# Kernel tuning notes

Hardware: AMD Instinct MI355X
Metric: run time of the kernel (lower is better)

Reference implementation:

```python
import jax, jax.numpy as jnp
import numpy as np

E = 8        # num_experts
TOPK = 2     # num_experts_per_tok
H = 2048     # hidden_size
I = 1024     # intermediate_size (c_fc outputs 2*I because is_glu)
STD = 0.02


def setup_inputs() -> dict:
    key = jax.random.key(0)
    k1, k2, k3, k4 = jax.random.split(key, 4)
    return {
        "x": jax.random.normal(k1, (4, 2048, H), jnp.float32),
        "w_gate": jax.random.normal(k2, (E, H), jnp.float32) * STD,
        "w_fc": jax.random.normal(k3, (E, 2 * I, H), jnp.float32) * STD,
        "w_proj": jax.random.normal(k4, (E, H, I), jnp.float32) * STD,
    }


def reference(x, w_gate, w_fc, w_proj):
    orig_shape = x.shape
    xf = x.reshape(-1, H)                      # [T, H]
    T = xf.shape[0]

    # routing
    router_logits = xf @ w_gate.T              # [T, E]
    top_vals, top_idx = jax.lax.top_k(router_logits, TOPK)   # [T, K]
    router_weights = jax.nn.softmax(top_vals.astype(jnp.float32), axis=-1).astype(x.dtype)

    # combine weights: [T, E], zero for unselected experts (top-k indices are distinct)
    combine = jnp.zeros((T, E), x.dtype).at[jnp.arange(T)[:, None], top_idx].set(router_weights)

    # per-expert FFN; equivalent to sort/scatter grouped GEMM since unselected
    # tokens get zero combine weight. scan over the small fixed expert axis
    # keeps peak memory to one [T, 2I] intermediate.
    def body(y, ewc):
        wfc_e, wproj_e, c_e = ewc              # [2I,H], [H,I], [T]
        h = xf @ wfc_e.T                       # [T, 2I]
        a, b = jnp.split(h, 2, axis=-1)
        h = jax.nn.silu(a) * b                 # GLU: [T, I]
        y = y + c_e[:, None] * (h @ wproj_e.T)
        return y, None

    y0 = jnp.zeros_like(xf)
    y, _ = jax.lax.scan(body, y0, (w_fc, w_proj, combine.T))
    return y.reshape(orig_shape), router_logits
```

## Files before the change

kernel.cpp:

```cpp
#include <hip/hip_runtime.h>
#include <hip/hip_bf16.h>
#include <stdint.h>

#define T_TOK 8192
#define HID   2048
#define IM    1024
#define NE    8

typedef __attribute__((ext_vector_type(8))) short bf16x8;
typedef __attribute__((ext_vector_type(4))) float f32x4;

__device__ __forceinline__ void gload16(void* lds, const void* g) {
  __builtin_amdgcn_global_load_lds((const __attribute__((address_space(1))) char*)g,
                                   (__attribute__((address_space(3))) char*)lds, 16, 0, 0);
}

__device__ __forceinline__ ushort f2b(float f) {
  union { float f; uint32_t u; } c; c.f = f;
  uint32_t u = c.u;
  return (ushort)((u + 0x7FFFu + ((u >> 16) & 1u)) >> 16);
}

#define MFMA16(a, b, c) __builtin_amdgcn_mfma_f32_16x16x32_bf16((a), (b), (c), 0, 0, 0)

__global__ void cast_w_kernel(const float* __restrict__ wfc, const float* __restrict__ wproj,
                              ushort* __restrict__ wfcb, ushort* __restrict__ wpb) {
  const int NFC4 = NE * 2 * IM * HID / 4;
  const int NPJ4 = NE * HID * IM / 4;
  int i = blockIdx.x * blockDim.x + threadIdx.x;
  int stride = gridDim.x * blockDim.x;
  for (; i < NFC4 + NPJ4; i += stride) {
    const float4* s; ushort4* d; int k;
    if (i < NFC4) { s = (const float4*)wfc;   d = (ushort4*)wfcb; k = i; }
    else          { s = (const float4*)wproj; d = (ushort4*)wpb;  k = i - NFC4; }
    float4 v = s[k];
    ushort4 o;
    o.x = f2b(v.x); o.y = f2b(v.y); o.z = f2b(v.z); o.w = f2b(v.w);
    d[k] = o;
  }
}

__global__ __launch_bounds__(256) void router_kernel(
    const float* __restrict__ x, const float* __restrict__ wg,
    float* __restrict__ logits_out, ushort* __restrict__ xb,
    int4* __restrict__ recI, float2* __restrict__ recW,
    int* __restrict__ counts2) {
  int wid = threadIdx.x >> 6, lane = threadIdx.x & 63;
  int tok = blockIdx.x * 4 + wid;
  if (tok >= T_TOK) return;
  const float4* xr = (const float4*)(x + (size_t)tok * HID);
  float4 xv[8];
#pragma unroll
  for (int j = 0; j < 8; ++j) xv[j] = xr[j * 64 + lane];
  ushort4* xbr = (ushort4*)(xb + (size_t)tok * HID);
#pragma unroll
  for (int j = 0; j < 8; ++j) {
    ushort4 o;
    o.x = f2b(xv[j].x); o.y = f2b(xv[j].y); o.z = f2b(xv[j].z); o.w = f2b(xv[j].w);
    xbr[j * 64 + lane] = o;
  }
  float lf[NE];
#pragma unroll
  for (int e = 0; e < NE; ++e) {
    const float4* wrow = (const float4*)(wg + (size_t)e * HID);
    double acc = 0.0;
#pragma unroll
    for (int j = 0; j < 8; ++j) {
      float4 w4 = wrow[j * 64 + lane];
      acc += (double)xv[j].x * w4.x + (double)xv[j].y * w4.y +
             (double)xv[j].z * w4.z + (double)xv[j].w * w4.w;
    }
#pragma unroll
    for (int off = 32; off; off >>= 1) acc += __shfl_xor(acc, off);
    lf[e] = (float)acc;
  }
  if (lane == 0) {
#pragma unroll
    for (int e = 0; e < NE; ++e) logits_out[(size_t)tok * NE + e] = lf[e];
    int i1 = 0;
#pragma unroll
    for (int e = 1; e < NE; ++e) if (lf[e] > lf[i1]) i1 = e;
    int i2 = -1;
#pragma unroll
    for (int e = 0; e < NE; ++e) {
      if (e == i1) continue;
      if (i2 < 0 || lf[e] > lf[i2]) i2 = e;
    }
    float t = expf(lf[i2] - lf[i1]);
    float w1 = 1.0f / (1.0f + t);
    float w2 = t / (1.0f + t);
    int s1 = atomicAdd(&counts2[i1 * 2 + 0], 1);
    int s2 = atomicAdd(&counts2[i2 * 2 + 1], 1);
    recI[tok] = make_int4(i1, s1, i2, s2);
    recW[tok] = make_float2(w1, w2);
  }
}

__global__ void scan_kernel(const int* __restrict__ counts2, int* __restrict__ offs2,
                            int* __restrict__ ecnt, int* __restrict__ eoff) {
  int s = 0;
  for (int b = 0; b < 2 * NE; ++b) { offs2[b] = s; s += counts2[b]; }
  offs2[2 * NE] = s;
  for (int e = 0; e < NE; ++e) {
    eoff[e] = offs2[2 * e];
    ecnt[e] = counts2[2 * e] + counts2[2 * e + 1];
  }
}

__global__ void scatter_kernel(const int4* __restrict__ recI, const float2* __restrict__ recW,
                               const int* __restrict__ offs2,
                               int* __restrict__ tok_id, float* __restrict__ aw) {
  int t = blockIdx.x * blockDim.x + threadIdx.x;
  if (t >= T_TOK) return;
  int4 r = recI[t]; float2 w = recW[t];
  int p1 = offs2[r.x * 2 + 0] + r.y; tok_id[p1] = t; aw[p1] = w.x;
  int p2 = offs2[r.z * 2 + 1] + r.w; tok_id[p2] = t; aw[p2] = w.y;
}


__global__ __launch_bounds__(512, 2) void gemm1_kernel(
    const ushort* __restrict__ xb, const ushort* __restrict__ wfcb,
    const int* __restrict__ tok_id, const float* __restrict__ aw,
    const int* __restrict__ ecnt, const int* __restrict__ eoff,
    ushort* __restrict__ hglu) {
  int bid = blockIdx.x;
  int e = bid >> 9;
  int rt = (bid >> 3) & 63;
  int ct = bid & 7;
  int cnt = ecnt[e];
  if (cnt == 0 || rt * 256 >= cnt) return;
  int off = eoff[e];
  int tid = threadIdx.x;

  __shared__ ushort lds[4][512 * 32];

  int sslot[4]; const ushort* gsrc[4];
#pragma unroll
  for (int l = 0; l < 4; ++l) {
    int s = l * 512 + tid;
    int lrow = s >> 2, qs = s & 3;
    int gq = qs ^ ((lrow >> 1) & 3);
    sslot[l] = s * 8;
    if (l < 2) {
      int slotr = rt * 256 + lrow;
      if (slotr >= cnt) slotr = cnt - 1;
      gsrc[l] = xb + (size_t)tok_id[off + slotr] * HID + gq * 8;
    } else if (l == 2) {
      int fcr = e * 2048 + ct * 128 + (lrow - 256);
      gsrc[l] = wfcb + (size_t)fcr * HID + gq * 8;
    } else {
      int fcr = e * 2048 + 1024 + ct * 128 + (lrow - 384);
      gsrc[l] = wfcb + (size_t)fcr * HID + gq * 8;
    }
  }

  int wid = tid >> 6, lane = tid & 63;
  int wr = wid >> 2, wc = wid & 3;
  int q = lane >> 4, r = lane & 15;

  int offA[8], offBa[2], offBb[2];
#pragma unroll
  for (int m = 0; m < 8; ++m) {
    int lrow = wr * 128 + m * 16 + r;
    offA[m] = lrow * 32 + ((q ^ ((lrow >> 1) & 3)) << 3);
  }
#pragma unroll
  for (int n = 0; n < 2; ++n) {
    int lr1 = 256 + wc * 32 + n * 16 + r;
    offBa[n] = lr1 * 32 + ((q ^ ((lr1 >> 1) & 3)) << 3);
    int lr2 = 384 + wc * 32 + n * 16 + r;
    offBb[n] = lr2 * 32 + ((q ^ ((lr2 >> 1) & 3)) << 3);
  }

  f32x4 accA[8][2] = {}; f32x4 accB[8][2] = {};
  const int NT = HID / 32;

#define G1_STAGE(bufi, t, l) gload16(&lds[bufi][sslot[l]], gsrc[l] + (size_t)(t) * 32)
#pragma unroll
  for (int t = 0; t < 3; ++t) {
    G1_STAGE(t, t, 0); G1_STAGE(t, t, 1); G1_STAGE(t, t, 2); G1_STAGE(t, t, 3);
  }
  asm volatile("s_waitcnt vmcnt(8)" ::: "memory");
  __builtin_amdgcn_s_barrier();

  for (int t = 0; t < NT; ++t) {
    int cur = t & 3;
    const ushort* Bv = &lds[cur][0];
    int nb = (t + 3) & 3;
    bool pf = (t + 3) < NT;
    bf16x8 ba0 = *(const bf16x8*)&Bv[offBa[0]];
    bf16x8 ba1 = *(const bf16x8*)&Bv[offBa[1]];
    bf16x8 bb0 = *(const bf16x8*)&Bv[offBb[0]];
    bf16x8 bb1 = *(const bf16x8*)&Bv[offBb[1]];
    bf16x8 af[4];
#pragma unroll
    for (int m = 0; m < 4; ++m) af[m] = *(const bf16x8*)&Bv[offA[m]];
    if (pf) { G1_STAGE(nb, t + 3, 0); G1_STAGE(nb, t + 3, 1); }
    __builtin_amdgcn_s_barrier();
    __builtin_amdgcn_s_setprio(1);
#pragma unroll
    for (int m = 0; m < 4; ++m) {
      accA[m][0] = MFMA16(af[m], ba0, accA[m][0]);
      accA[m][1] = MFMA16(af[m], ba1, accA[m][1]);
      accB[m][0] = MFMA16(af[m], bb0, accB[m][0]);
      accB[m][1] = MFMA16(af[m], bb1, accB[m][1]);
    }
    __builtin_amdgcn_s_setprio(0);
    __builtin_amdgcn_s_barrier();
#pragma unroll
    for (int m = 0; m < 4; ++m) af[m] = *(const bf16x8*)&Bv[offA[4 + m]];
    if (pf) { G1_STAGE(nb, t + 3, 2); G1_STAGE(nb, t + 3, 3); }
    __builtin_amdgcn_s_barrier();
    __builtin_amdgcn_s_setprio(1);
#pragma unroll
    for (int m = 0; m < 4; ++m) {
      accA[4 + m][0] = MFMA16(af[m], ba0, accA[4 + m][0]);
      accA[4 + m][1] = MFMA16(af[m], ba1, accA[4 + m][1]);
      accB[4 + m][0] = MFMA16(af[m], bb0, accB[4 + m][0]);
      accB[4 + m][1] = MFMA16(af[m], bb1, accB[4 + m][1]);
    }
    __builtin_amdgcn_s_setprio(0);
    if (t < NT - 1) {
      if (t + 3 < NT)      asm volatile("s_waitcnt vmcnt(8)" ::: "memory");
      else if (t + 2 < NT) asm volatile("s_waitcnt vmcnt(4)" ::: "memory");
      else                 asm volatile("s_waitcnt vmcnt(0)" ::: "memory");
      __builtin_amdgcn_s_barrier();
    }
  }

#pragma unroll
  for (int m = 0; m < 8; ++m) {
#pragma unroll
    for (int j = 0; j < 4; ++j) {
      int slot = rt * 256 + wr * 128 + m * 16 + q * 4 + j;
      if (slot >= cnt) continue;
      float w = aw[off + slot];
      size_t rp = (size_t)(off + slot) * IM + ct * 128 + wc * 32 + r;
#pragma unroll
      for (int n = 0; n < 2; ++n) {
        float a = accA[m][n][j], b = accB[m][n][j];
        float g = (a / (1.0f + expf(-a))) * b * w;
        hglu[rp + n * 16] = f2b(g);
      }
    }
  }
}

__global__ __launch_bounds__(512, 2) void gemm2_kernel(
    const ushort* __restrict__ hglu, const ushort* __restrict__ wpb,
    const int* __restrict__ tok_id,
    const int* __restrict__ counts2, const int* __restrict__ offs2,
    float* __restrict__ y, int pass) {
  int bid = blockIdx.x;
  int e = bid >> 8;
  int rt = (bid >> 3) & 31;
  int ct = bid & 7;
  int cnt = counts2[2 * e + pass];
  if (cnt == 0 || rt * 256 >= cnt) return;
  int off = offs2[2 * e + pass];
  int tid = threadIdx.x;

  __shared__ ushort lds[4][512 * 32];

  int sslot[4]; const ushort* gsrc[4];
#pragma unroll
  for (int l = 0; l < 4; ++l) {
    int s = l * 512 + tid;
    int lrow = s >> 2, qs = s & 3;
    int gq = qs ^ ((lrow >> 1) & 3);
    sslot[l] = s * 8;
    if (l < 2) {
      size_t arow = (size_t)(off + rt * 256 + lrow);
      gsrc[l] = hglu + arow * IM + gq * 8;
    } else {
      int wrow = e * 2048 + ct * 256 + (lrow - 256);
      gsrc[l] = wpb + (size_t)wrow * IM + gq * 8;
    }
  }

  int wid = tid >> 6, lane = tid & 63;
  int wr = wid >> 2, wc = wid & 3;
  int q = lane >> 4, r = lane & 15;

  int offA[8], offB[4];
#pragma unroll
  for (int m = 0; m < 8; ++m) {
    int lrow = wr * 128 + m * 16 + r;
    offA[m] = lrow * 32 + ((q ^ ((lrow >> 1) & 3)) << 3);
  }
#pragma unroll
  for (int n = 0; n < 4; ++n) {
    int lrow = 256 + wc * 64 + n * 16 + r;
    offB[n] = lrow * 32 + ((q ^ ((lrow >> 1) & 3)) << 3);
  }

  f32x4 acc[8][4] = {};
  const int NT = IM / 32;

#define G2_STAGE(bufi, t, l) gload16(&lds[bufi][sslot[l]], gsrc[l] + (size_t)(t) * 32)
#pragma unroll
  for (int t = 0; t < 3; ++t) {
    G2_STAGE(t, t, 0); G2_STAGE(t, t, 1); G2_STAGE(t, t, 2); G2_STAGE(t, t, 3);
  }
  asm volatile("s_waitcnt vmcnt(8)" ::: "memory");
  __builtin_amdgcn_s_barrier();

  for (int t = 0; t < NT; ++t) {
    int cur = t & 3;
    const ushort* Bv = &lds[cur][0];
    int nb = (t + 3) & 3;
    bool pf = (t + 3) < NT;
    bf16x8 bf0 = *(const bf16x8*)&Bv[offB[0]];
    bf16x8 bf1 = *(const bf16x8*)&Bv[offB[1]];
    bf16x8 bf2 = *(const bf16x8*)&Bv[offB[2]];
    bf16x8 bf3 = *(const bf16x8*)&Bv[offB[3]];
    bf16x8 af[4];
#pragma unroll
    for (int m = 0; m < 4; ++m) af[m] = *(const bf16x8*)&Bv[offA[m]];
    if (pf) { G2_STAGE(nb, t + 3, 0); G2_STAGE(nb, t + 3, 1); }
    __builtin_amdgcn_s_barrier();
    __builtin_amdgcn_s_setprio(1);
#pragma unroll
    for (int m = 0; m < 4; ++m) {
      acc[m][0] = MFMA16(af[m], bf0, acc[m][0]);
      acc[m][1] = MFMA16(af[m], bf1, acc[m][1]);
      acc[m][2] = MFMA16(af[m], bf2, acc[m][2]);
      acc[m][3] = MFMA16(af[m], bf3, acc[m][3]);
    }
    __builtin_amdgcn_s_setprio(0);
    __builtin_amdgcn_s_barrier();
#pragma unroll
    for (int m = 0; m < 4; ++m) af[m] = *(const bf16x8*)&Bv[offA[4 + m]];
    if (pf) { G2_STAGE(nb, t + 3, 2); G2_STAGE(nb, t + 3, 3); }
    __builtin_amdgcn_s_barrier();
    __builtin_amdgcn_s_setprio(1);
#pragma unroll
    for (int m = 0; m < 4; ++m) {
      acc[4 + m][0] = MFMA16(af[m], bf0, acc[4 + m][0]);
      acc[4 + m][1] = MFMA16(af[m], bf1, acc[4 + m][1]);
      acc[4 + m][2] = MFMA16(af[m], bf2, acc[4 + m][2]);
      acc[4 + m][3] = MFMA16(af[m], bf3, acc[4 + m][3]);
    }
    __builtin_amdgcn_s_setprio(0);
    if (t < NT - 1) {
      if (t + 3 < NT)      asm volatile("s_waitcnt vmcnt(8)" ::: "memory");
      else if (t + 2 < NT) asm volatile("s_waitcnt vmcnt(4)" ::: "memory");
      else                 asm volatile("s_waitcnt vmcnt(0)" ::: "memory");
      __builtin_amdgcn_s_barrier();
    }
  }

#pragma unroll
  for (int m = 0; m < 8; ++m) {
#pragma unroll
    for (int j = 0; j < 4; ++j) {
      int slot = rt * 256 + wr * 128 + m * 16 + q * 4 + j;
      if (slot >= cnt) continue;
      int tok = tok_id[off + slot];
      float* yp = &y[(size_t)tok * HID + ct * 256 + wc * 64 + r];
      if (pass == 0) {
#pragma unroll
        for (int n = 0; n < 4; ++n) yp[n * 16] = acc[m][n][j];
      } else {
#pragma unroll
        for (int n = 0; n < 4; ++n) yp[n * 16] += acc[m][n][j];
      }
    }
  }
}

extern "C" void kernel_launch(void* const* d_in, const int* in_sizes, int n_in,
                              void* d_out, int out_size, void* d_ws, size_t ws_size,
                              hipStream_t stream) {
  const float* x     = (const float*)d_in[0];
  const float* wg    = (const float*)d_in[1];
  const float* wfc   = (const float*)d_in[2];
  const float* wproj = (const float*)d_in[3];
  float* y = (float*)d_out;
  float* logits = y + (size_t)T_TOK * HID;

  char* ws = (char*)d_ws;
  ushort* xb    = (ushort*)(ws + 0);
  ushort* wfcb  = (ushort*)(ws + 33554432);
  ushort* wpb   = (ushort*)(ws + 100663296);
  ushort* hglu  = (ushort*)(ws + 134217728);
  int*    tok   = (int*)   (ws + 168296448);
  float*  aw    = (float*) (ws + 168361984);
  int4*   recI  = (int4*)  (ws + 168427520);
  float2* recW  = (float2*)(ws + 168558592);
  int* counts2  = (int*)   (ws + 168624128);
  int* offs2    = (int*)   (ws + 168624192);
  int* ecnt     = (int*)   (ws + 168624264);
  int* eoff     = (int*)   (ws + 168624296);
  if (ws_size < 168624328) return;

  hipMemsetAsync(counts2, 0, 2 * NE * sizeof(int), stream);

  cast_w_kernel<<<4096, 256, 0, stream>>>(wfc, wproj, wfcb, wpb);
  router_kernel<<<T_TOK / 4, 256, 0, stream>>>(x, wg, logits, xb, recI, recW, counts2);
  scan_kernel<<<1, 1, 0, stream>>>(counts2, offs2, ecnt, eoff);
  scatter_kernel<<<(T_TOK + 255) / 256, 256, 0, stream>>>(recI, recW, offs2, tok, aw);

  gemm1_kernel<<<NE * 64 * 8, 512, 0, stream>>>(xb, wfcb, tok, aw, ecnt, eoff, hglu);
  gemm2_kernel<<<NE * 32 * 8, 512, 0, stream>>>(hglu, wpb, tok, counts2, offs2, y, 0);
  gemm2_kernel<<<NE * 32 * 8, 512, 0, stream>>>(hglu, wpb, tok, counts2, offs2, y, 1);
}
```

Baseline: 844.5 us.

## Shrink gemm2 tiles to 128x128 with double buffering and warp-parallel scan

Rewrites the down-projection GEMM to use 128x128 output tiles with 256 threads and a simple two-stage LDS double buffer, replacing the 256x256 tile, 4-stage pipeline with split barriers and priority hints. This makes the grid finer so partially filled expert row tiles waste less work and more blocks can spread across CUs. In exchange each tile gets less operand reuse and global loads overlap less with compute. The single-thread scan kernel is also replaced by a wavefront shuffle prefix sum.

```diff
diff --git a/kernel.cpp b/kernel.cpp
--- a/kernel.cpp
+++ b/kernel.cpp
@@ -98,13 +98,21 @@
 
 __global__ void scan_kernel(const int* __restrict__ counts2, int* __restrict__ offs2,
                             int* __restrict__ ecnt, int* __restrict__ eoff) {
-  int s = 0;
-  for (int b = 0; b < 2 * NE; ++b) { offs2[b] = s; s += counts2[b]; }
-  offs2[2 * NE] = s;
-  for (int e = 0; e < NE; ++e) {
-    eoff[e] = offs2[2 * e];
-    ecnt[e] = counts2[2 * e] + counts2[2 * e + 1];
-  }
+  int lane = threadIdx.x;
+  int c = (lane < 2 * NE) ? counts2[lane] : 0;
+  int s = c;
+#pragma unroll
+  for (int d = 1; d < 16; d <<= 1) {
+    int v = __shfl_up(s, d);
+    if (lane >= d) s += v;
+  }
+  int excl = s - c;
+  if (lane < 2 * NE) offs2[lane] = excl;
+  if (lane == 2 * NE - 1) offs2[2 * NE] = s;
+  int e2a = __shfl(excl, (lane & 7) * 2);
+  int ca  = __shfl(c, (lane & 7) * 2);
+  int cb  = __shfl(c, (lane & 7) * 2 + 1);
+  if (lane < NE) { eoff[lane] = e2a; ecnt[lane] = ca + cb; }
 }
 
 __global__ void scatter_kernel(const int4* __restrict__ recI, const float2* __restrict__ recW,
@@ -246,118 +254,89 @@
   }
 }
 
-__global__ __launch_bounds__(512, 2) void gemm2_kernel(
+__global__ __launch_bounds__(256, 2) void gemm2_kernel(
     const ushort* __restrict__ hglu, const ushort* __restrict__ wpb,
     const int* __restrict__ tok_id,
     const int* __restrict__ counts2, const int* __restrict__ offs2,
     float* __restrict__ y, int pass) {
   int bid = blockIdx.x;
-  int e = bid >> 8;
-  int rt = (bid >> 3) & 31;
-  int ct = bid & 7;
+  int e = bid >> 10;
+  int rem = bid & 1023;
+  int rt = rem >> 4;
+  int ct = rem & 15;
   int cnt = counts2[2 * e + pass];
-  if (cnt == 0 || rt * 256 >= cnt) return;
+  if (cnt == 0 || rt * 128 >= cnt) return;
   int off = offs2[2 * e + pass];
   int tid = threadIdx.x;
 
-  __shared__ ushort lds[4][512 * 32];
-
-  int sslot[4]; const ushort* gsrc[4];
-#pragma unroll
-  for (int l = 0; l < 4; ++l) {
-    int s = l * 512 + tid;
-    int lrow = s >> 2, qs = s & 3;
-    int gq = qs ^ ((lrow >> 1) & 3);
-    sslot[l] = s * 8;
-    if (l < 2) {
-      size_t arow = (size_t)(off + rt * 256 + lrow);
-      gsrc[l] = hglu + arow * IM + gq * 8;
-    } else {
-      int wrow = e * 2048 + ct * 256 + (lrow - 256);
-      gsrc[l] = wpb + (size_t)wrow * IM + gq * 8;
-    }
+  __shared__ ushort As[2][128 * 32];
+  __shared__ ushort Bs[2][128 * 32];
+
+  const ushort* gA[2]; const ushort* gB[2];
+  int sslot[2];
+#pragma unroll
+  for (int p = 0; p < 2; ++p) {
+    int s = p * 256 + tid;
+    int row = s >> 2, qs = s & 3;
+    int gq = qs ^ ((row >> 1) & 3);
+    sslot[p] = s * 8;
+    gA[p] = hglu + (size_t)(off + rt * 128 + row) * IM + gq * 8;
+    gB[p] = wpb + (size_t)(e * 2048 + ct * 128 + row) * IM + gq * 8;
   }
 
   int wid = tid >> 6, lane = tid & 63;
-  int wr = wid >> 2, wc = wid & 3;
+  int wr = wid >> 1, wc = wid & 1;
   int q = lane >> 4, r = lane & 15;
 
-  int offA[8], offB[4];
-#pragma unroll
-  for (int m = 0; m < 8; ++m) {
-    int lrow = wr * 128 + m * 16 + r;
-    offA[m] = lrow * 32 + ((q ^ ((lrow >> 1) & 3)) << 3);
+  int offA[4], offB[4];
+#pragma unroll
+  for (int m = 0; m < 4; ++m) {
+    int row = wr * 64 + m * 16 + r;
+    offA[m] = row * 32 + ((q ^ ((row >> 1) & 3)) << 3);
   }
 #pragma unroll
   for (int n = 0; n < 4; ++n) {
-    int lrow = 256 + wc * 64 + n * 16 + r;
-    offB[n] = lrow * 32 + ((q ^ ((lrow >> 1) & 3)) << 3);
-  }
-
-  f32x4 acc[8][4] = {};
+    int row = wc * 64 + n * 16 + r;
+    offB[n] = row * 32 + ((q ^ ((row >> 1) & 3)) << 3);
+  }
+
+  f32x4 acc[4][4] = {};
   const int NT = IM / 32;
 
-#define G2_STAGE(bufi, t, l) gload16(&lds[bufi][sslot[l]], gsrc[l] + (size_t)(t) * 32)
-#pragma unroll
-  for (int t = 0; t < 3; ++t) {
-    G2_STAGE(t, t, 0); G2_STAGE(t, t, 1); G2_STAGE(t, t, 2); G2_STAGE(t, t, 3);
-  }
-  asm volatile("s_waitcnt vmcnt(8)" ::: "memory");
-  __builtin_amdgcn_s_barrier();
-
-  for (int t = 0; t < NT; ++t) {
-    int cur = t & 3;
-    const ushort* Bv = &lds[cur][0];
-    int nb = (t + 3) & 3;
-    bool pf = (t + 3) < NT;
-    bf16x8 bf0 = *(const bf16x8*)&Bv[offB[0]];
-    bf16x8 bf1 = *(const bf16x8*)&Bv[offB[1]];
-    bf16x8 bf2 = *(const bf16x8*)&Bv[offB[2]];
-    bf16x8 bf3 = *(const bf16x8*)&Bv[offB[3]];
-    bf16x8 af[4];
-#pragma unroll
-    for (int m = 0; m < 4; ++m) af[m] = *(const bf16x8*)&Bv[offA[m]];
-    if (pf) { G2_STAGE(nb, t + 3, 0); G2_STAGE(nb, t + 3, 1); }
-    __builtin_amdgcn_s_barrier();
-    __builtin_amdgcn_s_setprio(1);
-#pragma unroll
-    for (int m = 0; m < 4; ++m) {
-      acc[m][0] = MFMA16(af[m], bf0, acc[m][0]);
-      acc[m][1] = MFMA16(af[m], bf1, acc[m][1]);
-      acc[m][2] = MFMA16(af[m], bf2, acc[m][2]);
-      acc[m][3] = MFMA16(af[m], bf3, acc[m][3]);
-    }
-    __builtin_amdgcn_s_setprio(0);
-    __builtin_amdgcn_s_barrier();
-#pragma unroll
-    for (int m = 0; m < 4; ++m) af[m] = *(const bf16x8*)&Bv[offA[4 + m]];
-    if (pf) { G2_STAGE(nb, t + 3, 2); G2_STAGE(nb, t + 3, 3); }
-    __builtin_amdgcn_s_barrier();
-    __builtin_amdgcn_s_setprio(1);
-#pragma unroll
-    for (int m = 0; m < 4; ++m) {
-      acc[4 + m][0] = MFMA16(af[m], bf0, acc[4 + m][0]);
-      acc[4 + m][1] = MFMA16(af[m], bf1, acc[4 + m][1]);
-      acc[4 + m][2] = MFMA16(af[m], bf2, acc[4 + m][2]);
-      acc[4 + m][3] = MFMA16(af[m], bf3, acc[4 + m][3]);
-    }
-    __builtin_amdgcn_s_setprio(0);
-    if (t < NT - 1) {
-      if (t + 3 < NT)      asm volatile("s_waitcnt vmcnt(8)" ::: "memory");
-      else if (t + 2 < NT) asm volatile("s_waitcnt vmcnt(4)" ::: "memory");
-      else                 asm volatile("s_waitcnt vmcnt(0)" ::: "memory");
-      __builtin_amdgcn_s_barrier();
-    }
-  }
-
-#pragma unroll
-  for (int m = 0; m < 8; ++m) {
+  auto stage = [&](int b, int kt) {
+#pragma unroll
+    for (int p = 0; p < 2; ++p) {
+      gload16(&As[b][sslot[p]], gA[p] + (size_t)kt * 32);
+      gload16(&Bs[b][sslot[p]], gB[p] + (size_t)kt * 32);
+    }
+  };
+
+  stage(0, 0);
+  __syncthreads();
+  for (int kt = 0; kt < NT; ++kt) {
+    int cur = kt & 1;
+    if (kt < NT - 1) stage(cur ^ 1, kt + 1);
+    bf16x8 af[4], bf[4];
+#pragma unroll
+    for (int m = 0; m < 4; ++m) af[m] = *(const bf16x8*)&As[cur][offA[m]];
+#pragma unroll
+    for (int n = 0; n < 4; ++n) bf[n] = *(const bf16x8*)&Bs[cur][offB[n]];
+#pragma unroll
+    for (int m = 0; m < 4; ++m)
+#pragma unroll
+      for (int n = 0; n < 4; ++n)
+        acc[m][n] = MFMA16(af[m], bf[n], acc[m][n]);
+    __syncthreads();
+  }
+
+#pragma unroll
+  for (int m = 0; m < 4; ++m) {
 #pragma unroll
     for (int j = 0; j < 4; ++j) {
-      int slot = rt * 256 + wr * 128 + m * 16 + q * 4 + j;
+      int slot = rt * 128 + wr * 64 + m * 16 + q * 4 + j;
       if (slot >= cnt) continue;
       int tok = tok_id[off + slot];
-      float* yp = &y[(size_t)tok * HID + ct * 256 + wc * 64 + r];
+      float* yp = &y[(size_t)tok * HID + ct * 128 + wc * 64 + r];
       if (pass == 0) {
 #pragma unroll
         for (int n = 0; n < 4; ++n) yp[n * 16] = acc[m][n][j];
@@ -398,10 +377,10 @@
 
   cast_w_kernel<<<4096, 256, 0, stream>>>(wfc, wproj, wfcb, wpb);
   router_kernel<<<T_TOK / 4, 256, 0, stream>>>(x, wg, logits, xb, recI, recW, counts2);
-  scan_kernel<<<1, 1, 0, stream>>>(counts2, offs2, ecnt, eoff);
+  scan_kernel<<<1, 64, 0, stream>>>(counts2, offs2, ecnt, eoff);
   scatter_kernel<<<(T_TOK + 255) / 256, 256, 0, stream>>>(recI, recW, offs2, tok, aw);
 
   gemm1_kernel<<<NE * 64 * 8, 512, 0, stream>>>(xb, wfcb, tok, aw, ecnt, eoff, hglu);
-  gemm2_kernel<<<NE * 32 * 8, 512, 0, stream>>>(hglu, wpb, tok, counts2, offs2, y, 0);
-  gemm2_kernel<<<NE * 32 * 8, 512, 0, stream>>>(hglu, wpb, tok, counts2, offs2, y, 1);
-}
+  gemm2_kernel<<<NE * 64 * 16, 256, 0, stream>>>(hglu, wpb, tok, counts2, offs2, y, 0);
+  gemm2_kernel<<<NE * 64 * 16, 256, 0, stream>>>(hglu, wpb, tok, counts2, offs2, y, 1);
+}
```

Measured after the change: 814.1 us. -3.6%, faster.
